# Kernel tuning notes

Hardware: AMD Instinct MI355X
Metric: run time of the kernel (lower is better)

The kernel has to match this reference:

```python
import jax, jax.numpy as jnp
import numpy as np
import math

# batch, in-channels, attention_maps, heads, features (== input height), frames
B, C, M, H, F_, W = 2, 8, 8, 8, 256, 512
HD = F_ // H  # head dim = 32


def conv2d(x, w, pad):
    return jax.lax.conv_general_dilated(x, w, (1, 1), pad,
                                        dimension_numbers=('NCHW', 'OIHW', 'NCHW'))


def rotary(x):
    # lucidrains-style interleaved rotary over last dim; x: [..., seq, d]
    d, seq = x.shape[-1], x.shape[-2]
    inv_freq = 1.0 / (10000.0 ** (jnp.arange(0, d, 2, dtype=jnp.float32) / d))
    freqs = jnp.arange(seq, dtype=jnp.float32)[:, None] * inv_freq[None, :]  # [seq, d/2]
    freqs = jnp.repeat(freqs, 2, axis=-1)  # [seq, d], each freq repeated for the (x1,x2) pair
    cos, sin = jnp.cos(freqs), jnp.sin(freqs)
    x1, x2 = x[..., 0::2], x[..., 1::2]
    xr = jnp.stack((-x2, x1), axis=-1).reshape(x.shape)  # rotate_half
    return x * cos + xr * sin


def setup_inputs() -> dict:
    key = jax.random.key(0)
    ks = jax.random.split(key, 12)
    s = 0.02
    return {
        'x': jax.random.normal(ks[0], (B, C, F_, W), jnp.float32),
        'prev_qk': jax.random.normal(ks[1], (B, M, H, W, W), jnp.float32) * 0.1,
        'q_c1': jax.random.normal(ks[2], (M, C, 3, 3), jnp.float32) * s,
        'q_lin': jax.random.normal(ks[3], (M, F_, F_), jnp.float32) * s,
        'q_c2': jax.random.normal(ks[4], (M, M, 1, 3), jnp.float32) * s,
        'k_c1': jax.random.normal(ks[5], (M, C, 3, 3), jnp.float32) * s,
        'k_lin': jax.random.normal(ks[6], (M, F_, F_), jnp.float32) * s,
        'k_c2': jax.random.normal(ks[7], (M, M, 1, 3), jnp.float32) * s,
        'v_c1': jax.random.normal(ks[8], (M, C, 3, 3), jnp.float32) * s,
        'v_lin': jax.random.normal(ks[9], (M, F_, F_), jnp.float32) * s,
        'v_c2': jax.random.normal(ks[10], (M, M, 1, 3), jnp.float32) * s,
        'o_w': jax.random.normal(ks[11], (M, F_, F_), jnp.float32) * s,
    }


def _proj(x, wc1, wl, wc2):
    h = conv2d(x, wc1, [(1, 1), (1, 1)])        # [B,M,F,W] 3x3 conv, no bias
    h = jnp.einsum('bcfw,cgf->bcgw', h, wl)      # MultichannelLinear: per-map linear on feature dim
    h = conv2d(h, wc2, [(0, 0), (1, 1)])         # (1,3) conv along frames
    return h


def _heads(t):
    # [B,M,F,W] -> transpose(2,3) -> [B,M,W,F] -> [B,M,W,H,HD] -> [B,M,H,W,HD]
    return t.transpose(0, 1, 3, 2).reshape(B, M, W, H, HD).transpose(0, 1, 3, 2, 4)


def reference(x, prev_qk, q_c1, q_lin, q_c2, k_c1, k_lin, k_c2, v_c1, v_lin, v_c2, o_w):
    q = rotary(_heads(_proj(x, q_c1, q_lin, q_c2)))
    k = rotary(_heads(_proj(x, k_c1, k_lin, k_c2)))
    v = _heads(_proj(x, v_c1, v_lin, v_c2))
    # scaled by sqrt(h) where h == input height == features (non-standard)
    qk = jnp.einsum('bmhqd,bmhkd->bmhqk', q, k) / math.sqrt(F_) + prev_qk
    a = jnp.einsum('bmhqk,bmhkd->bmhqd', jax.nn.softmax(qk, axis=-1), v)
    a = a.transpose(0, 1, 3, 2, 4).reshape(B, M, W, F_).transpose(0, 1, 3, 2)  # [B,M,F,W]
    out = jnp.einsum('bcfw,cgf->bcgw', a, o_w)  # o_proj MultichannelLinear
    return (out, qk)
```

## Files before the change

kernel.cpp:

```cpp
#include <hip/hip_runtime.h>

#define B 2
#define C 8
#define M 8
#define H 8
#define F 256
#define W 512
#define HD 32

typedef __attribute__((ext_vector_type(8))) __bf16 bf16x8;
typedef __attribute__((ext_vector_type(4))) float f32x4;

__device__ __forceinline__ unsigned short f2bf(float f) {
    unsigned int u = __float_as_uint(f);
    return (unsigned short)((u + 0x7fffu + ((u >> 16) & 1u)) >> 16);
}

__global__ __launch_bounds__(256) void conv1_kernel(const float* __restrict__ x,
                                                    const float* __restrict__ w0,
                                                    const float* __restrict__ w1,
                                                    const float* __restrict__ w2,
                                                    float* __restrict__ out) {
    __shared__ float wl[72];
    int t = threadIdx.x;
    int z = blockIdx.z;
    int proj = z >> 4, bz = z & 15;
    int b = bz >> 3, m = bz & 7;
    const float* wt = (proj == 0) ? w0 : (proj == 1) ? w1 : w2;
    if (t < 72) wl[t] = wt[m * 72 + t];
    __syncthreads();
    int f = blockIdx.y;
    int w = blockIdx.x * 256 + t;
    const float* xb = x + (size_t)b * C * F * W;
    float acc = 0.f;
    for (int i = 0; i < 8; ++i) {
        const float* xi = xb + (size_t)i * F * W;
        #pragma unroll
        for (int df = 0; df < 3; ++df) {
            int ff = f + df - 1;
            if (ff < 0 || ff >= F) continue;
            const float* xr = xi + (size_t)ff * W;
            float v0 = (w - 1 >= 0) ? xr[w - 1] : 0.f;
            float v1 = xr[w];
            float v2 = (w + 1 < W) ? xr[w + 1] : 0.f;
            const float* wr = &wl[(i * 3 + df) * 3];
            acc += v0 * wr[0] + v1 * wr[1] + v2 * wr[2];
        }
    }
    out[((size_t)z * F + f) * W + w] = acc;
}

__global__ __launch_bounds__(256) void lin_kernel(const float* __restrict__ in,
                                                  const float* __restrict__ w0,
                                                  const float* __restrict__ w1,
                                                  const float* __restrict__ w2,
                                                  float* __restrict__ out) {
    __shared__ float As[32][68];
    __shared__ float Bs[32][68];
    int t = threadIdx.x;
    int z = blockIdx.z;
    int proj = z >> 4, m = z & 7;
    const float* wsel = (proj == 0) ? w0 : (proj == 1) ? w1 : w2;
    const float* wm = wsel + (size_t)m * F * F;
    const float* ib = in + (size_t)z * F * W;
    float* ob = out + (size_t)z * F * W;
    int g0 = blockIdx.y * 64, wb0 = blockIdx.x * 64;
    int ty = t >> 4, tx = t & 15;
    int gg = t >> 2, fq = (t & 3) * 8;
    int lkk = t >> 3, wq = (t & 7) * 8;
    float4 a0 = *(const float4*)&wm[(size_t)(g0 + gg) * F + fq];
    float4 a1 = *(const float4*)&wm[(size_t)(g0 + gg) * F + fq + 4];
    float4 b0 = *(const float4*)&ib[(size_t)lkk * W + wb0 + wq];
    float4 b1 = *(const float4*)&ib[(size_t)lkk * W + wb0 + wq + 4];
    float acc[4][4] = {};
    for (int f0 = 0; f0 < F; f0 += 32) {
        As[fq + 0][gg] = a0.x; As[fq + 1][gg] = a0.y; As[fq + 2][gg] = a0.z; As[fq + 3][gg] = a0.w;
        As[fq + 4][gg] = a1.x; As[fq + 5][gg] = a1.y; As[fq + 6][gg] = a1.z; As[fq + 7][gg] = a1.w;
        *(float4*)&Bs[lkk][wq] = b0;
        *(float4*)&Bs[lkk][wq + 4] = b1;
        __syncthreads();
        if (f0 + 32 < F) {
            a0 = *(const float4*)&wm[(size_t)(g0 + gg) * F + f0 + 32 + fq];
            a1 = *(const float4*)&wm[(size_t)(g0 + gg) * F + f0 + 32 + fq + 4];
            b0 = *(const float4*)&ib[(size_t)(f0 + 32 + lkk) * W + wb0 + wq];
            b1 = *(const float4*)&ib[(size_t)(f0 + 32 + lkk) * W + wb0 + wq + 4];
        }
        #pragma unroll
        for (int kk = 0; kk < 32; ++kk) {
            float4 a4 = *(const float4*)&As[kk][ty * 4];
            float4 b4 = *(const float4*)&Bs[kk][tx * 4];
            acc[0][0] += a4.x * b4.x; acc[0][1] += a4.x * b4.y; acc[0][2] += a4.x * b4.z; acc[0][3] += a4.x * b4.w;
            acc[1][0] += a4.y * b4.x; acc[1][1] += a4.y * b4.y; acc[1][2] += a4.y * b4.z; acc[1][3] += a4.y * b4.w;
            acc[2][0] += a4.z * b4.x; acc[2][1] += a4.z * b4.y; acc[2][2] += a4.z * b4.z; acc[2][3] += a4.z * b4.w;
            acc[3][0] += a4.w * b4.x; acc[3][1] += a4.w * b4.y; acc[3][2] += a4.w * b4.z; acc[3][3] += a4.w * b4.w;
        }
        __syncthreads();
    }
    #pragma unroll
    for (int i = 0; i < 4; ++i) {
        float4 o = make_float4(acc[i][0], acc[i][1], acc[i][2], acc[i][3]);
        *(float4*)&ob[(size_t)(g0 + ty * 4 + i) * W + wb0 + tx * 4] = o;
    }
}

__global__ __launch_bounds__(256) void conv2_heads_kernel(const float* __restrict__ in,
                                                          const float* __restrict__ w0c,
                                                          const float* __restrict__ w1c,
                                                          const float* __restrict__ w2c,
                                                          unsigned short* __restrict__ outp) {
    __shared__ float wl[192];
    __shared__ float Ot[64][65];
    int t = threadIdx.x;
    int z = blockIdx.z;
    int proj = z >> 4, bz = z & 15;
    int b = bz >> 3, o = bz & 7;
    const float* wt = (proj == 0) ? w0c : (proj == 1) ? w1c : w2c;
    int do_rot = (proj < 2);
    if (t < 192) wl[t] = wt[t];
    __syncthreads();
    int f0 = blockIdx.y * 64, w0 = blockIdx.x * 64;
    const float* ib = in + ((size_t)proj * 16 + (size_t)b * M) * F * W;
    int ww = t & 63, fq = (t >> 6) * 16;
    int w = w0 + ww;
    for (int ff = 0; ff < 16; ++ff) {
        int f = f0 + fq + ff;
        float acc = 0.f;
        #pragma unroll
        for (int i = 0; i < 8; ++i) {
            const float* r = ib + ((size_t)i * F + f) * W + w;
            float v0 = (w - 1 >= 0) ? r[-1] : 0.f;
            float v1 = r[0];
            float v2 = (w + 1 < W) ? r[1] : 0.f;
            const float* wr = &wl[(o * 8 + i) * 3];
            acc += v0 * wr[0] + v1 * wr[1] + v2 * wr[2];
        }
        Ot[fq + ff][ww] = acc;
    }
    __syncthreads();
    size_t zbase = (size_t)z * H * W * HD;
    if (do_rot) {
        for (int k = 0; k < 16; ++k) {
            int idx = k * 256 + t;
            int ddh = idx & 63;
            int wi = idx >> 6;
            int f = f0 + ddh;
            int h = f >> 5, d = f & 31;
            float e  = Ot[ddh & ~1][wi];
            float od = Ot[ddh | 1][wi];
            int jp = d >> 1;
            float invf = exp2f(-(float)jp * 0.83048202372184058f);
            float th = (float)(w0 + wi) * invf;
            float cs = __cosf(th), sn = __sinf(th);
            float val = (d & 1) ? (od * cs + e * sn) : (e * cs - od * sn);
            outp[zbase + ((size_t)h * W + (w0 + wi)) * HD + d] = f2bf(val);
        }
    } else {
        for (int k = 0; k < 16; ++k) {
            int idx = k * 256 + t;
            int wi = idx & 63;
            int ddh = idx >> 6;
            int f = f0 + ddh;
            int h = f >> 5, d = f & 31;
            outp[zbase + ((size_t)(h * HD + d)) * W + (w0 + wi)] = f2bf(Ot[ddh][wi]);
        }
    }
}

__global__ __launch_bounds__(256) void attn_kernel(const unsigned short* __restrict__ qb,
                                                   const unsigned short* __restrict__ kb,
                                                   const unsigned short* __restrict__ vtb,
                                                   const float* __restrict__ prev,
                                                   float* __restrict__ qk,
                                                   float* __restrict__ abuf) {
    __shared__ __align__(16) unsigned short VsT[32 * 520];
    __shared__ __align__(16) unsigned short PT[4][16 * 72];
    int t = threadIdx.x;
    int l = t & 63, wv = t >> 6;
    int lr = l & 15, lg = l >> 4;
    int w0 = blockIdx.x * 64;
    int bmh = blockIdx.y;
    const unsigned short* Q  = qb  + (size_t)bmh * W * HD;
    const unsigned short* K  = kb  + (size_t)bmh * W * HD;
    const unsigned short* VT = vtb + (size_t)bmh * HD * W;
    const float* P0 = prev + (size_t)bmh * W * W;
    float* QK = qk + (size_t)bmh * W * W;
    int bm = bmh >> 3, h = bmh & 7;
    float* A = abuf + ((size_t)bm * F + h * HD) * W;

    #pragma unroll
    for (int it = 0; it < 8; ++it) {
        int e16 = it * 256 + t;
        int hd = e16 >> 6, w8 = (e16 & 63) * 8;
        *(uint4*)&VsT[hd * 520 + w8] = *(const uint4*)&VT[(size_t)hd * W + w8];
    }
    int qrow = w0 + wv * 16;
    bf16x8 qf = *(const bf16x8*)&Q[(size_t)(qrow + lr) * HD + lg * 8];

    float m_i[4], l_i[4];
    f32x4 accA[2];
    #pragma unroll
    for (int r = 0; r < 4; ++r) { m_i[r] = -3.0e38f; l_i[r] = 0.f; }
    accA[0] = (f32x4)0.f;
    accA[1] = (f32x4)0.f;

    __syncthreads();

    bf16x8 kfA[4], kfB[4];
    f32x4 pvA[4], pvB[4];

    auto issue = [&](bf16x8 (&kf)[4], f32x4 (&pv)[4], int c) {
        int j0 = c * 64;
        #pragma unroll
        for (int ct = 0; ct < 4; ++ct)
            kf[ct] = *(const bf16x8*)&K[(size_t)(j0 + ct * 16 + lr) * HD + lg * 8];
        #pragma unroll
        for (int ct = 0; ct < 4; ++ct) {
            const float* pr = &P0[(size_t)(qrow + lg * 4) * W + j0 + ct * 16 + lr];
            #pragma unroll
            for (int r = 0; r < 4; ++r) pv[ct][r] = pr[(size_t)r * W];
        }
    };

    auto step = [&](bf16x8 (&kf)[4], f32x4 (&pv)[4], int c) {
        int j0 = c * 64;
        f32x4 sc[4];
        #pragma unroll
        for (int ct = 0; ct < 4; ++ct)
            sc[ct] = __builtin_amdgcn_mfma_f32_16x16x32_bf16(qf, kf[ct], pv[ct] * 16.f, 0, 0, 0);
        float sv[4][4];
        #pragma unroll
        for (int ct = 0; ct < 4; ++ct) {
            #pragma unroll
            for (int r = 0; r < 4; ++r) {
                sv[ct][r] = sc[ct][r] * 0.0625f;
                QK[(size_t)(qrow + lg * 4 + r) * W + j0 + ct * 16 + lr] = sv[ct][r];
            }
        }
        float p[4][4];
        #pragma unroll
        for (int r = 0; r < 4; ++r) {
            float cm = fmaxf(fmaxf(sv[0][r], sv[1][r]), fmaxf(sv[2][r], sv[3][r]));
            #pragma unroll
            for (int off = 1; off < 16; off <<= 1) cm = fmaxf(cm, __shfl_xor(cm, off));
            float mn = fmaxf(m_i[r], cm);
            float alpha = __expf(m_i[r] - mn);
            m_i[r] = mn;
            float rs = 0.f;
            #pragma unroll
            for (int ct = 0; ct < 4; ++ct) { p[ct][r] = __expf(sv[ct][r] - mn); rs += p[ct][r]; }
            #pragma unroll
            for (int off = 1; off < 16; off <<= 1) rs += __shfl_xor(rs, off);
            l_i[r] = l_i[r] * alpha + rs;
            accA[0][r] *= alpha;
            accA[1][r] *= alpha;
        }
        unsigned short* PTw = &PT[wv][0];
        #pragma unroll
        for (int ct = 0; ct < 4; ++ct)
            #pragma unroll
            for (int r = 0; r < 4; ++r)
                PTw[(lg * 4 + r) * 72 + ct * 16 + lr] = f2bf(p[ct][r]);
        asm volatile("s_waitcnt lgkmcnt(0)" ::: "memory");
        __builtin_amdgcn_sched_barrier(0);
        bf16x8 pf[2];
        pf[0] = *(const bf16x8*)&PTw[lr * 72 + lg * 8];
        pf[1] = *(const bf16x8*)&PTw[lr * 72 + 32 + lg * 8];
        #pragma unroll
        for (int ks = 0; ks < 2; ++ks)
            #pragma unroll
            for (int ct2 = 0; ct2 < 2; ++ct2) {
                bf16x8 vf = *(const bf16x8*)&VsT[(ct2 * 16 + lr) * 520 + j0 + ks * 32 + lg * 8];
                accA[ct2] = __builtin_amdgcn_mfma_f32_16x16x32_bf16(pf[ks], vf, accA[ct2], 0, 0, 0);
            }
    };

    issue(kfA, pvA, 0);
    #pragma unroll
    for (int cc = 0; cc < 4; ++cc) {
        issue(kfB, pvB, 2 * cc + 1);
        step(kfA, pvA, 2 * cc);
        if (cc < 3) issue(kfA, pvA, 2 * cc + 2);
        step(kfB, pvB, 2 * cc + 1);
    }

    float inv[4];
    #pragma unroll
    for (int r = 0; r < 4; ++r) inv[r] = 1.f / l_i[r];
    float* Otf = (float*)&PT[wv][0];
    asm volatile("s_waitcnt lgkmcnt(0)" ::: "memory");
    #pragma unroll
    for (int ct2 = 0; ct2 < 2; ++ct2)
        #pragma unroll
        for (int r = 0; r < 4; ++r)
            Otf[(lg * 4 + r) * 33 + ct2 * 16 + lr] = accA[ct2][r] * inv[r];
    asm volatile("s_waitcnt lgkmcnt(0)" ::: "memory");
    __builtin_amdgcn_sched_barrier(0);
    #pragma unroll
    for (int k = 0; k < 8; ++k) {
        int flat = k * 64 + l;
        int woff = flat & 15, d = flat >> 4;
        A[(size_t)d * W + w0 + wv * 16 + woff] = Otf[woff * 33 + d];
    }
}

extern "C" void kernel_launch(void* const* d_in, const int* in_sizes, int n_in,
                              void* d_out, int out_size, void* d_ws, size_t ws_size,
                              hipStream_t stream) {
    const float* x    = (const float*)d_in[0];
    const float* prev = (const float*)d_in[1];
    const float* qc1  = (const float*)d_in[2];
    const float* qlin = (const float*)d_in[3];
    const float* qc2  = (const float*)d_in[4];
    const float* kc1  = (const float*)d_in[5];
    const float* klin = (const float*)d_in[6];
    const float* kc2  = (const float*)d_in[7];
    const float* vc1  = (const float*)d_in[8];
    const float* vlin = (const float*)d_in[9];
    const float* vc2  = (const float*)d_in[10];
    const float* ow   = (const float*)d_in[11];
    float* out0  = (float*)d_out;
    float* qkout = out0 + (size_t)B * M * F * W;
    float* ws = (float*)d_ws;
    size_t n = (size_t)B * M * F * W;
    float* r1 = ws;
    float* r2 = ws + 3 * n;
    unsigned short* qkv16 = (unsigned short*)r1;

    dim3 blk(256);
    dim3 gconv1(2, 256, 48), glin3(8, 4, 48), gconv2(8, 4, 48);
    dim3 gattn(8, 128), glin1(8, 4, 16);

    conv1_kernel<<<gconv1, blk, 0, stream>>>(x, qc1, kc1, vc1, r1);
    lin_kernel<<<glin3, blk, 0, stream>>>(r1, qlin, klin, vlin, r2);
    conv2_heads_kernel<<<gconv2, blk, 0, stream>>>(r2, qc2, kc2, vc2, qkv16);
    attn_kernel<<<gattn, blk, 0, stream>>>(qkv16, qkv16 + n, qkv16 + 2 * n, prev, qkout, r2);
    lin_kernel<<<glin1, blk, 0, stream>>>(r2, ow, ow, ow, out0);
}
```

Before: 438.2 us.

## Register-tile conv1 over 8 rows and fuse Q/K/V weight sets per thread

The 3x3 conv kernel now has each thread compute 8 consecutive feature rows for all three projections. It loads a 10-row input window into registers once per input channel and reuses it across rows and across the Q/K/V filters. This cuts redundant global loads of x, which was previously reread by 48 separate block groups and 3 rows per output. The cost is higher register pressure, uniform weight loads from global memory instead of shared memory, and a smaller grid of 1024 blocks.

Result: faster. 410.5 us (-6.3%).

```diff
diff --git a/kernel.cpp b/kernel.cpp
--- a/kernel.cpp
+++ b/kernel.cpp
@@ -21,33 +21,56 @@
                                                     const float* __restrict__ w1,
                                                     const float* __restrict__ w2,
                                                     float* __restrict__ out) {
-    __shared__ float wl[72];
     int t = threadIdx.x;
-    int z = blockIdx.z;
-    int proj = z >> 4, bz = z & 15;
-    int b = bz >> 3, m = bz & 7;
-    const float* wt = (proj == 0) ? w0 : (proj == 1) ? w1 : w2;
-    if (t < 72) wl[t] = wt[m * 72 + t];
-    __syncthreads();
-    int f = blockIdx.y;
-    int w = blockIdx.x * 256 + t;
+    int zb = blockIdx.z;
+    int b = zb >> 3, m = zb & 7;
+    int wi = blockIdx.x * 64 + (t & 63);
+    int f0t = blockIdx.y * 32 + (t >> 6) * 8;
     const float* xb = x + (size_t)b * C * F * W;
-    float acc = 0.f;
+    const float* wq = w0 + m * 72;
+    const float* wk = w1 + m * 72;
+    const float* wv = w2 + m * 72;
+    int wm = (wi > 0) ? wi - 1 : 0;
+    int wp = (wi < W - 1) ? wi + 1 : W - 1;
+    bool e0 = (wi > 0), e1 = (wi < W - 1);
+    float acc[3][8] = {};
     for (int i = 0; i < 8; ++i) {
         const float* xi = xb + (size_t)i * F * W;
-        #pragma unroll
-        for (int df = 0; df < 3; ++df) {
-            int ff = f + df - 1;
-            if (ff < 0 || ff >= F) continue;
-            const float* xr = xi + (size_t)ff * W;
-            float v0 = (w - 1 >= 0) ? xr[w - 1] : 0.f;
-            float v1 = xr[w];
-            float v2 = (w + 1 < W) ? xr[w + 1] : 0.f;
-            const float* wr = &wl[(i * 3 + df) * 3];
-            acc += v0 * wr[0] + v1 * wr[1] + v2 * wr[2];
-        }
-    }
-    out[((size_t)z * F + f) * W + w] = acc;
+        float v0[10], v1[10], v2[10];
+        #pragma unroll
+        for (int rr = 0; rr < 10; ++rr) {
+            int ff = f0t + rr - 1;
+            if (ff >= 0 && ff < F) {
+                const float* xr = xi + (size_t)ff * W;
+                float a = xr[wm], bb = xr[wi], c = xr[wp];
+                v0[rr] = e0 ? a : 0.f;
+                v1[rr] = bb;
+                v2[rr] = e1 ? c : 0.f;
+            } else {
+                v0[rr] = 0.f; v1[rr] = 0.f; v2[rr] = 0.f;
+            }
+        }
+        #pragma unroll
+        for (int p = 0; p < 3; ++p) {
+            const float* wt = ((p == 0) ? wq : (p == 1) ? wk : wv) + i * 9;
+            #pragma unroll
+            for (int df = 0; df < 3; ++df) {
+                float s0 = wt[df * 3 + 0];
+                float s1 = wt[df * 3 + 1];
+                float s2 = wt[df * 3 + 2];
+                #pragma unroll
+                for (int ff = 0; ff < 8; ++ff)
+                    acc[p][ff] += v0[ff + df] * s0 + v1[ff + df] * s1 + v2[ff + df] * s2;
+            }
+        }
+    }
+    #pragma unroll
+    for (int p = 0; p < 3; ++p) {
+        size_t zo = (size_t)(p * 16 + zb) * F;
+        #pragma unroll
+        for (int ff = 0; ff < 8; ++ff)
+            out[(zo + f0t + ff) * W + wi] = acc[p][ff];
+    }
 }
 
 __global__ __launch_bounds__(256) void lin_kernel(const float* __restrict__ in,
@@ -327,7 +350,7 @@
     unsigned short* qkv16 = (unsigned short*)r1;
 
     dim3 blk(256);
-    dim3 gconv1(2, 256, 48), glin3(8, 4, 48), gconv2(8, 4, 48);
+    dim3 gconv1(8, 8, 16), glin3(8, 4, 48), gconv2(8, 4, 48);
     dim3 gattn(8, 128), glin1(8, 4, 16);
 
     conv1_kernel<<<gconv1, blk, 0, stream>>>(x, qc1, kc1, vc1, r1);
```
